# Kernel optimization log

Hardware: AMD Instinct MI355X
Metric: run time of the kernel (lower is better)

Reference implementation:

```python
import jax, jax.numpy as jnp
import numpy as np

K = 3; STRIDE = 1; PAD = 1
IN_C = 256; OUT_C = 512
M = 5; TABLE_SIZE = 16
D = K * K * IN_C  # 2304


def _P(v, m):
    # ALSH preprocessing transform: append norm powers ||v||^2, ||v||^4, ...
    n2 = jnp.sum(v * v)
    powers = jnp.stack([n2 ** (2 ** i) for i in range(m)])
    return jnp.concatenate([v, powers])


def _Q(v, m):
    # ALSH query transform: append m halves
    return jnp.concatenate([v, jnp.full((m,), 0.5, v.dtype)])


def _hash_index(a, v):
    # hf followed by fmod(table_size).abs() as in the torch module
    h = jnp.floor(jnp.dot(a, v))
    return jnp.abs(jnp.mod(h, TABLE_SIZE)).astype(jnp.int32)


def _im2col(x):
    # x: (N, C, H, W) -> (K*K*C, N*h2*w2), rows ordered (kh, kw, c) to match
    # the (out, k, k, in) kernel flattening of the original module.
    N, C, H, W = x.shape
    h2 = (H - K + 2 * PAD) // STRIDE + 1
    w2 = (W - K + 2 * PAD) // STRIDE + 1
    xp = jnp.pad(x, ((0, 0), (0, 0), (PAD, PAD), (PAD, PAD)))
    cols = []
    for i in range(K):          # small fixed loop (k*k = 9)
        for j in range(K):
            cols.append(xp[:, :, i:i + h2 * STRIDE:STRIDE, j:j + w2 * STRIDE:STRIDE])
    p = jnp.stack(cols, 0)                 # (K*K, N, C, h2, w2)
    p = p.transpose(0, 2, 1, 3, 4)         # (K*K, C, N, h2, w2)
    return p.reshape(K * K * C, N * h2 * w2), h2, w2


def setup_inputs() -> dict:
    key = jax.random.key(0)
    k1, k2, k3, k4 = jax.random.split(key, 4)
    stdv = 1.0 / np.sqrt(IN_C * K * K)
    x = jax.random.normal(k1, (16, IN_C, 56, 56), dtype=jnp.float32)
    kernels = jax.random.uniform(k2, (OUT_C, D), dtype=jnp.float32,
                                 minval=-stdv, maxval=stdv)
    bias = jax.random.uniform(k3, (1, OUT_C, 1, 1), dtype=jnp.float32,
                              minval=-stdv, maxval=stdv)
    a = jax.random.normal(k4, (D + M,), dtype=jnp.float32)
    return {"x": x, "kernels": kernels, "bias": bias, "a": a, "mode": 0}


def reference(x, kernels, bias, a, mode):
    N = x.shape[0]
    patch_matr, h2, w2 = _im2col(x)  # (D, N*h2*w2)

    # --- build ALSH table: hash index per kernel row (non-differentiable) ---
    kernel_idx = jax.lax.stop_gradient(
        jax.vmap(lambda kr: _hash_index(a, _P(kr, M)))(kernels))  # (OUT_C,)

    # --- query: max over each patch row, normalized to unit vector ---
    max_row = patch_matr.max(axis=1)                    # (D,)
    unit = max_row / jnp.linalg.norm(max_row)
    q_idx = jax.lax.stop_gradient(_hash_index(a, _Q(unit, M)))

    # --- routed subset matmul, expressed as a row mask (jit-safe) ---
    mask = (kernel_idx == q_idx)                        # (OUT_C,) bool
    count = mask.sum()
    full = kernels @ patch_matr                         # (OUT_C, N*h2*w2)
    scale = jnp.where(count > 0, count / OUT_C, 1.0).astype(full.dtype)
    out = jnp.where(count > 0,
                    jnp.where(mask[:, None], full, 0.0) / scale,
                    full)

    out = out.reshape(OUT_C, N, h2 * w2).transpose(1, 0, 2)
    out = out.reshape(N, OUT_C, h2, w2)
    return out + bias
```

## Files before the change

### kernel.cpp

```cpp
#include <hip/hip_runtime.h>
#include <math.h>

#define IN_C   256
#define OUT_C  512
#define HW     3136
#define W_     56
#define D_     2304
#define TBL    16


#define XB_OFF 2375680ULL
#define XB_ROW 1856

typedef __attribute__((ext_vector_type(8))) __bf16 bf16x8;
typedef __attribute__((ext_vector_type(4))) float f32x4;

__device__ __forceinline__ ushort f2bf(float f) {
  uint b = __float_as_uint(f);
  b = b + 0x7FFFu + ((b >> 16) & 1u);
  return (ushort)(b >> 16);
}

__global__ __launch_bounds__(256) void k_chanmax(const float* __restrict__ x,
                                                 float* __restrict__ ws) {
  int c = blockIdx.x, t = threadIdx.x;
  float m[3][3];
#pragma unroll
  for (int i = 0; i < 3; i++)
#pragma unroll
    for (int j = 0; j < 3; j++) m[i][j] = -INFINITY;

  for (int e = t; e < 16 * HW; e += 256) {
    int n = e / HW;
    int rem = e - n * HW;
    int r = rem / W_;
    int s = rem - r * W_;
    float v = x[(size_t)(n * IN_C + c) * HW + rem];
    bool rc[3] = { r <= 54, true, r >= 1 };
    bool sc[3] = { s <= 54, true, s >= 1 };
#pragma unroll
    for (int i = 0; i < 3; i++)
#pragma unroll
      for (int j = 0; j < 3; j++)
        if (rc[i] && sc[j]) m[i][j] = fmaxf(m[i][j], v);
  }
#pragma unroll
  for (int i = 0; i < 3; i++)
#pragma unroll
    for (int j = 0; j < 3; j++)
      for (int o = 32; o; o >>= 1)
        m[i][j] = fmaxf(m[i][j], __shfl_down(m[i][j], o, 64));

  __shared__ float red[4][9];
  int lane = t & 63, wid = t >> 6;
  if (lane == 0) {
#pragma unroll
    for (int i = 0; i < 3; i++)
#pragma unroll
      for (int j = 0; j < 3; j++) red[wid][i * 3 + j] = m[i][j];
  }
  __syncthreads();
  if (t < 9) {
    float v = fmaxf(fmaxf(red[0][t], red[1][t]), fmaxf(red[2][t], red[3][t]));
    int i = t / 3, j = t - i * 3;
    if (i != 1 || j != 1) v = fmaxf(v, 0.0f);
    ws[(size_t)t * IN_C + c] = v;
  }
}

__global__ __launch_bounds__(256) void k_qhash(const float* __restrict__ a,
                                               float* __restrict__ ws) {
  const float* max_row = ws;
  int t = threadIdx.x;
  double sd = 0.0, sq = 0.0;
  for (int d = t; d < D_; d += 256) {
    double v = (double)max_row[d];
    sd += (double)a[d] * v;
    sq += v * v;
  }
  __shared__ double sh[8], sh2[8];
  int lane = t & 63, wid = t >> 6;
  for (int o = 32; o; o >>= 1) {
    sd += __shfl_down(sd, o, 64);
    sq += __shfl_down(sq, o, 64);
  }
  if (lane == 0) { sh[wid] = sd; sh2[wid] = sq; }
  __syncthreads();
  if (t == 0) {
    double td = 0, tq = 0;
    for (int w = 0; w < 4; w++) { td += sh[w]; tq += sh2[w]; }
    double dot = td / sqrt(tq);
    dot += 0.5 * ((double)a[D_] + (double)a[D_ + 1] + (double)a[D_ + 2] +
                  (double)a[D_ + 3] + (double)a[D_ + 4]);
    long long h = (long long)floor(dot);
    ((int*)ws)[2816] = (int)((h % TBL + TBL) % TBL);
  }
}

__global__ __launch_bounds__(256) void k_khash(const float* __restrict__ kern,
                                               const float* __restrict__ a,
                                               float* __restrict__ ws) {
  int o = blockIdx.x, t = threadIdx.x;
  const float* kr = kern + (size_t)o * D_;
  double sd = 0, sn = 0;
  for (int d = t; d < D_; d += 256) {
    double w = (double)kr[d];
    sd += (double)a[d] * w;
    sn += w * w;
  }
  __shared__ double sh[8], sh2[8];
  int lane = t & 63, wid = t >> 6;
  for (int off = 32; off; off >>= 1) {
    sd += __shfl_down(sd, off, 64);
    sn += __shfl_down(sn, off, 64);
  }
  if (lane == 0) { sh[wid] = sd; sh2[wid] = sn; }
  __syncthreads();
  if (t == 0) {
    double td = 0, tn = 0;
    for (int w = 0; w < 4; w++) { td += sh[w]; tn += sh2[w]; }
    double p1 = tn, p2 = p1 * p1, p4 = p2 * p2, p8 = p4 * p4, p16 = p8 * p8;
    td += (double)a[D_] * p1 + (double)a[D_ + 1] * p2 + (double)a[D_ + 2] * p4 +
          (double)a[D_ + 3] * p8 + (double)a[D_ + 4] * p16;
    long long h = (long long)floor(td);
    ((int*)ws)[2304 + o] = (int)((h % TBL + TBL) % TBL);
  }
}

__global__ __launch_bounds__(512) void k_select(float* __restrict__ ws) {
  int t = threadIdx.x;
  int* hashk = (int*)ws + 2304;
  int* qidx = (int*)ws + 2816;
  int* cntp = (int*)ws + 2817;
  float* scalep = ws + 2818;
  int* active = (int*)ws + 2819;
  int* flags = (int*)ws + 3331;
  __shared__ int cnt;
  if (t == 0) cnt = 0;
  active[t] = 0;
  __syncthreads();
  int q = *qidx;
  bool m = (hashk[t] == q);
  if (m) {
    int p = atomicAdd(&cnt, 1);
    active[p] = t;
  }
  __syncthreads();
  int c = cnt;
  flags[t] = (c == 0) ? 1 : (m ? 1 : 0);
  if (c == 0) active[t] = t;
  if (t == 0) {
    if (c > 0) { *cntp = c; *scalep = 512.0f / (float)c; }
    else       { *cntp = 512; *scalep = 1.0f; }
  }
}

__global__ __launch_bounds__(256) void k_prep(const float* __restrict__ kern,
                                              float* __restrict__ ws) {
  const int* iws = (const int*)ws;
  int cnt = iws[2817];
  const int* active = iws + 2819;
  ushort* Wc = (ushort*)((char*)ws + 16384);
  int s = blockIdx.x, t = threadIdx.x;
  if (s < cnt) {
    int oc = active[s];
    const float* src = kern + (size_t)oc * D_;
    for (int e = t; e < D_; e += 256) Wc[(size_t)s * D_ + e] = f2bf(src[e]);
  } else {
    for (int e = t; e < D_; e += 256) Wc[(size_t)s * D_ + e] = 0;
  }
}

__global__ __launch_bounds__(256) void k_xprep(const float* __restrict__ x,
                                               float* __restrict__ ws) {
  ushort* xb = (ushort*)((char*)ws + XB_OFF);
  int bx = blockIdx.x;
  int n = bx & 15, yp = bx >> 4;
  int t = threadIdx.x;
  const size_t CGS = (size_t)16 * 58 * XB_ROW;
  size_t rb0 = (size_t)(n * 58 + yp) * XB_ROW;
  uint4 z4 = make_uint4(0u, 0u, 0u, 0u);

  if (yp == 0 || yp == 57) {
    for (int e = t; e < 8 * 232; e += 256) {
      int cg = e / 232, k = e - cg * 232;
      *(uint4*)&xb[rb0 + (size_t)cg * CGS + (size_t)k * 8] = z4;
    }
    return;
  }
  if (t < 64) {
    int cg = t >> 3, r = t & 7;
    int wp = (r >> 2) ? 57 : 0;
    int oct = r & 3;
    *(uint4*)&xb[rb0 + (size_t)cg * CGS + wp * 32 + oct * 8] = z4;
  }
  int y = yp - 1;
  __shared__ float Lf[64 * 57];
  for (int c0 = 0; c0 < 256; c0 += 64) {
    __syncthreads();
    for (int e = t; e < 3584; e += 256) {
      int ci = e / 56, w = e - ci * 56;
      Lf[ci * 57 + w] = x[(size_t)(n * 256 + c0 + ci) * 3136 + y * 56 + w];
    }
    __syncthreads();
    for (int e = t; e < 448; e += 256) {
      int w = e >> 3, cg_l = (e >> 2) & 1, oct = e & 3;
      int cb = cg_l * 32 + oct * 8;
      uint pk[4];
#pragma unroll
      for (int k = 0; k < 4; k++) {
        uint lo = f2bf(Lf[(cb + 2 * k) * 57 + w]);
        uint hi = f2bf(Lf[(cb + 2 * k + 1) * 57 + w]);
        pk[k] = lo | (hi << 16);
      }
      int cg = (c0 >> 5) + cg_l;
      *(uint4*)&xb[rb0 + (size_t)cg * CGS + (w + 1) * 32 + oct * 8] =
          make_uint4(pk[0], pk[1], pk[2], pk[3]);
    }
  }
}

__global__ __launch_bounds__(256) void k_biasfill(const float* __restrict__ bias,
                                                  const float* __restrict__ ws,
                                                  float* __restrict__ out) {
  const int* flags = (const int*)ws + 3331;
  const int total4 = 16 * OUT_C * HW / 4;
  int stride = gridDim.x * blockDim.x;
  for (int i = blockIdx.x * blockDim.x + threadIdx.x; i < total4; i += stride) {
    int o = (i / 784) & (OUT_C - 1);
    if (!flags[o]) {
      float b = bias[o];
      ((float4*)out)[i] = make_float4(b, b, b, b);
    }
  }
}

#define XSTR 40
#define ASTR 40
#define XSTRIDE 40
#define ASTRIDE 104

__global__ __launch_bounds__(256, 2) void k_convx(const float* __restrict__ bias,
                                                  const float* __restrict__ ws,
                                                  float* __restrict__ out) {
  const int* iws = (const int*)ws;
  int cnt = iws[2817];
  int octile = blockIdx.y;
  if (octile * 128 >= cnt) return;
  float sc = ws[2818];
  const int* active = iws + 2819;
  const ushort* Wc = (const ushort*)((const char*)ws + 16384);
  const ushort* xb = (const ushort*)((const char*)ws + XB_OFF);

  int rt = blockIdx.x;
  int n = blockIdx.z;
  int t = threadIdx.x;
  int lane = t & 63, wid = t >> 6;
  int quad = lane >> 4, l16 = lane & 15;
  int ochalf = wid & 1, pxhalf = wid >> 1;

  __shared__ __align__(16) ushort X_lds[2][348 * XSTR];
  __shared__ __align__(16) ushort A_lds[2][128 * ASTR];

  int pbase[7];
#pragma unroll
  for (int b = 0; b < 7; b++) {
    int pxl = pxhalf * 112 + b * 16 + l16;
    int rl = pxl / 56;
    int col = pxl - rl * 56;
    pbase[b] = ((rl + 1) * 58 + (col + 1)) * XSTR;
  }

  int ar0 = t >> 2;
  int aq = (t & 3) * 8;
  const ushort* Wrow0 = Wc + (size_t)(octile * 128 + ar0) * D_ + aq;
  const ushort* Wrow1 = Wrow0 + (size_t)64 * D_;
  int aoff0 = ar0 * ASTR + aq;
  int aoff1 = (ar0 + 64) * ASTR + aq;

  const size_t CGS = (size_t)16 * 58 * XB_ROW;
  const ushort* xsrc = xb + (size_t)(n * 58 + rt * 4) * XB_ROW;

  f32x4 acc[4][7];
#pragma unroll
  for (int a = 0; a < 4; a++)
#pragma unroll
    for (int b = 0; b < 7; b++) acc[a][b] = (f32x4){0.f, 0.f, 0.f, 0.f};

  {
    uint4 a0 = *(const uint4*)(Wrow0);
    uint4 a1 = *(const uint4*)(Wrow1);
    *(uint4*)&A_lds[0][aoff0] = a0;
    *(uint4*)&A_lds[0][aoff1] = a1;
    for (int j = t; j < 1392; j += 256)
      *(uint4*)&X_lds[0][(j >> 2) * XSTR + (j & 3) * 8] =
          *(const uint4*)(xsrc + (size_t)j * 8);
  }
  __syncthreads();

  for (int cc = 0; cc < 8; ++cc) {
    const int xc = cc & 1;
#pragma unroll
    for (int tap = 0; tap < 9; ++tap) {
      const int cur = (cc + tap) & 1;
      const bool havenext = !(cc == 7 && tap == 8);
      const int tapn = (tap == 8) ? 0 : tap + 1;
      const int ccn = (tap == 8) ? cc + 1 : cc;
      uint4 a0, a1, xv;
      if (havenext) {
        int goff = tapn * 256 + ccn * 32;
        a0 = *(const uint4*)(Wrow0 + goff);
        a1 = *(const uint4*)(Wrow1 + goff);
      }
      const bool xpf = (tap < 6) && (cc < 7) && (t < 232);
      int xj = tap * 232 + t;
      if (xpf)
        xv = *(const uint4*)(xsrc + (size_t)(cc + 1) * CGS + (size_t)xj * 8);

      const int kh = tap / 3, kw = tap - kh * 3;
      const int poff = ((kh - 1) * 58 + (kw - 1)) * XSTR + quad * 8;
      bf16x8 af[4];
#pragma unroll
      for (int a = 0; a < 4; a++) {
        union { uint4 u; bf16x8 v; } cv;
        cv.u = *(const uint4*)&A_lds[cur][(ochalf * 64 + a * 16 + l16) * ASTR +
                                          quad * 8];
        af[a] = cv.v;
      }
      __builtin_amdgcn_s_setprio(1);
#pragma unroll
      for (int b = 0; b < 7; b++) {
        union { uint4 u; bf16x8 v; } cv;
        cv.u = *(const uint4*)&X_lds[xc][pbase[b] + poff];
        bf16x8 xf = cv.v;
#pragma unroll
        for (int a = 0; a < 4; a++)
          acc[a][b] = __builtin_amdgcn_mfma_f32_16x16x32_bf16(af[a], xf,
                                                              acc[a][b], 0, 0, 0);
      }
      __builtin_amdgcn_s_setprio(0);

      if (havenext) {
        const int nxt = cur ^ 1;
        *(uint4*)&A_lds[nxt][aoff0] = a0;
        *(uint4*)&A_lds[nxt][aoff1] = a1;
      }
      if (xpf)
        *(uint4*)&X_lds[xc ^ 1][(xj >> 2) * XSTR + (xj & 3) * 8] = xv;
      __syncthreads();
    }
  }

  size_t nbase = (size_t)n * OUT_C * HW;
#pragma unroll
  for (int a = 0; a < 4; a++) {
#pragma unroll
    for (int r = 0; r < 4; r++) {
      int slot = octile * 128 + ochalf * 64 + a * 16 + quad * 4 + r;
      if (slot < cnt) {
        int oc = active[slot];
        float bv = bias[oc];
        size_t obase = nbase + (size_t)oc * HW + rt * 224 + pxhalf * 112 + l16;
#pragma unroll
        for (int b = 0; b < 7; b++)
          out[obase + b * 16] = acc[a][b][r] * sc + bv;
      }
    }
  }
}

__global__ __launch_bounds__(256, 2) void k_conv(const float* __restrict__ x,
                                                 const float* __restrict__ bias,
                                                 const float* __restrict__ ws,
                                                 float* __restrict__ out) {
  const int* iws = (const int*)ws;
  int cnt = iws[2817];
  int octile = blockIdx.y;
  if (octile * 128 >= cnt) return;
  float sc = ws[2818];
  const int* active = iws + 2819;
  const ushort* Wc = (const ushort*)((const char*)ws + 16384);

  int rt = blockIdx.x;
  int n = blockIdx.z;
  int t = threadIdx.x;
  int lane = t & 63, wid = t >> 6;
  int quad = lane >> 4, l16 = lane & 15;
  int ochalf = wid & 1, pxhalf = wid >> 1;

  __shared__ __align__(16) ushort X_lds[348 * XSTRIDE];
  __shared__ __align__(16) ushort A_lds[128 * ASTRIDE];

  const float* xin = x + (size_t)n * IN_C * HW;

  int pbase[7];
#pragma unroll
  for (int b = 0; b < 7; b++) {
    int pxl = pxhalf * 112 + b * 16 + l16;
    int rl = pxl / 56;
    int col = pxl - rl * 56;
    pbase[b] = ((rl + 1) * 58 + (col + 1)) * XSTRIDE;
  }

  f32x4 acc[4][7];
#pragma unroll
  for (int a = 0; a < 4; a++)
#pragma unroll
    for (int b = 0; b < 7; b++) acc[a][b] = (f32x4){0.f, 0.f, 0.f, 0.f};

  for (int cc = 0; cc < 8; ++cc) {
    int c0 = cc * 32;
    __syncthreads();
    for (int e = t; e < 1392; e += 256) {
      int q = e / 348;
      int p = e - q * 348;
      int rl = p / 58;
      int cp = p - rl * 58;
      int y = rt * 4 - 1 + rl;
      int xx = cp - 1;
      float vv[8];
      if ((unsigned)y < 56u && (unsigned)xx < 56u) {
        const float* src = xin + (size_t)(c0 + q * 8) * HW + y * W_ + xx;
#pragma unroll
        for (int k = 0; k < 8; k++) vv[k] = src[(size_t)k * HW];
      } else {
#pragma unroll
        for (int k = 0; k < 8; k++) vv[k] = 0.f;
      }
      uint4 pk;
      pk.x = (uint)f2bf(vv[0]) | ((uint)f2bf(vv[1]) << 16);
      pk.y = (uint)f2bf(vv[2]) | ((uint)f2bf(vv[3]) << 16);
      pk.z = (uint)f2bf(vv[4]) | ((uint)f2bf(vv[5]) << 16);
      pk.w = (uint)f2bf(vv[6]) | ((uint)f2bf(vv[7]) << 16);
      *(uint4*)&X_lds[p * XSTRIDE + q * 8] = pk;
    }

    for (int kh = 0; kh < 3; ++kh) {
      __syncthreads();
      for (int e = t; e < 1536; e += 256) {
        int oc = e / 12;
        int seg = e - oc * 12;
        int tl = seg >> 2, q = seg & 3;
        uint4 v = *(const uint4*)(Wc + (size_t)(octile * 128 + oc) * D_ +
                                  (kh * 3 + tl) * IN_C + c0 + q * 8);
        *(uint4*)&A_lds[oc * ASTRIDE + tl * 32 + q * 8] = v;
      }
      __syncthreads();

      int di = kh - 1;
#pragma unroll
      for (int djj = 0; djj < 3; ++djj) {
        int poff = (di * 58 + (djj - 1)) * XSTRIDE + quad * 8;
        bf16x8 bfr[7];
#pragma unroll
        for (int b = 0; b < 7; b++) {
          union { uint4 u; bf16x8 v; } cv;
          cv.u = *(const uint4*)&X_lds[pbase[b] + poff];
          bfr[b] = cv.v;
        }
#pragma unroll
        for (int a = 0; a < 4; a++) {
          union { uint4 u; bf16x8 v; } cv;
          cv.u = *(const uint4*)&A_lds[(ochalf * 64 + a * 16 + l16) * ASTRIDE +
                                       djj * 32 + quad * 8];
          bf16x8 af = cv.v;
#pragma unroll
          for (int b = 0; b < 7; b++)
            acc[a][b] = __builtin_amdgcn_mfma_f32_16x16x32_bf16(af, bfr[b],
                                                                acc[a][b], 0, 0, 0);
        }
      }
    }
  }

  size_t nbase = (size_t)n * OUT_C * HW;
#pragma unroll
  for (int a = 0; a < 4; a++) {
#pragma unroll
    for (int r = 0; r < 4; r++) {
      int slot = octile * 128 + ochalf * 64 + a * 16 + quad * 4 + r;
      if (slot < cnt) {
        int oc = active[slot];
        float bv = bias[oc];
        size_t obase = nbase + (size_t)oc * HW + rt * 224 + pxhalf * 112 + l16;
#pragma unroll
        for (int b = 0; b < 7; b++)
          out[obase + b * 16] = acc[a][b][r] * sc + bv;
      }
    }
  }
}

extern "C" void kernel_launch(void* const* d_in, const int* in_sizes, int n_in,
                              void* d_out, int out_size, void* d_ws, size_t ws_size,
                              hipStream_t stream) {
  const float* x    = (const float*)d_in[0];
  const float* kern = (const float*)d_in[1];
  const float* bias = (const float*)d_in[2];
  const float* a    = (const float*)d_in[3];
  float* out = (float*)d_out;
  float* ws  = (float*)d_ws;

  const size_t need = XB_OFF + (size_t)8 * 16 * 58 * 58 * 32 * 2;

  k_chanmax<<<dim3(IN_C), dim3(256), 0, stream>>>(x, ws);
  k_qhash<<<dim3(1), dim3(256), 0, stream>>>(a, ws);
  k_khash<<<dim3(OUT_C), dim3(256), 0, stream>>>(kern, a, ws);
  k_select<<<dim3(1), dim3(512), 0, stream>>>(ws);
  k_prep<<<dim3(OUT_C), dim3(256), 0, stream>>>(kern, ws);
  k_biasfill<<<dim3(4096), dim3(256), 0, stream>>>(bias, ws, out);
  if (ws_size >= need) {
    k_xprep<<<dim3(16 * 58), dim3(256), 0, stream>>>(x, ws);
    k_convx<<<dim3(14, 4, 16), dim3(256), 0, stream>>>(bias, ws, out);
  } else {
    k_conv<<<dim3(14, 4, 16), dim3(256), 0, stream>>>(x, bias, ws, out);
  }
}
```

Before: 371.4 us.

## Fuse setup kernels, fold bias fill into conv, deepen weight prefetch

Merges the x bf16 repack, the channel-max reduction (split across four batch parts) and the kernel hashing into one k_setup launch, and replaces the query hash and selection kernels with a single k_route kernel. The separate bias-fill pass over the whole output is removed; inactive output channels are now bias-filled inside k_convx by the otherwise idle octile blocks. The conv loop prefetches weights two taps ahead through registers and delays the X LDS store by one step, hiding global latency better. It also widens the k_prep bf16 stores. This cuts launch count and a full output write, at the cost of more register pressure in the conv kernel and extra workspace for the partial maxima.

```diff
diff --git a/kernel.cpp b/kernel.cpp
--- a/kernel.cpp
+++ b/kernel.cpp
@@ -11,6 +11,7 @@
 
 #define XB_OFF 2375680ULL
 #define XB_ROW 1856
+#define P_OFF  7483392
 
 typedef __attribute__((ext_vector_type(8))) __bf16 bf16x8;
 typedef __attribute__((ext_vector_type(4))) float f32x4;
@@ -21,6 +22,360 @@
   return (ushort)(b >> 16);
 }
 
+
+__global__ __launch_bounds__(256) void k_setup(const float* __restrict__ x,
+                                               const float* __restrict__ kern,
+                                               const float* __restrict__ a,
+                                               float* __restrict__ ws) {
+  __shared__ __align__(16) float smem[64 * 57];
+  int bx = blockIdx.x, t = threadIdx.x;
+
+  if (bx < 3712) {
+    int c0i = bx & 3;
+    int n = (bx >> 2) & 15;
+    int yp = bx >> 6;
+    int c0 = c0i * 64, cgbase = c0i * 2;
+    ushort* xb = (ushort*)((char*)ws + XB_OFF);
+    const size_t CGS = (size_t)16 * 58 * XB_ROW;
+    size_t rb0 = (size_t)(n * 58 + yp) * XB_ROW;
+    uint4 z4 = make_uint4(0u, 0u, 0u, 0u);
+
+    if (yp == 0 || yp == 57) {
+      for (int e = t; e < 464; e += 256) {
+        int cg_l = e / 232, k = e - cg_l * 232;
+        *(uint4*)&xb[rb0 + (size_t)(cgbase + cg_l) * CGS + (size_t)k * 8] = z4;
+      }
+      return;
+    }
+    if (t < 16) {
+      int cg_l = t >> 3, r = t & 7;
+      int wp = (r >> 2) ? 57 : 0, oct = r & 3;
+      *(uint4*)&xb[rb0 + (size_t)(cgbase + cg_l) * CGS + wp * 32 + oct * 8] = z4;
+    }
+    int y = yp - 1;
+    float* Lf = smem;
+    for (int e = t; e < 3584; e += 256) {
+      int ci = e / 56, w = e - ci * 56;
+      Lf[ci * 57 + w] = x[(size_t)(n * 256 + c0 + ci) * 3136 + y * 56 + w];
+    }
+    __syncthreads();
+    for (int e = t; e < 448; e += 256) {
+      int w = e >> 3, cg_l = (e >> 2) & 1, oct = e & 3;
+      int cb = cg_l * 32 + oct * 8;
+      uint pk[4];
+#pragma unroll
+      for (int k = 0; k < 4; k++) {
+        uint lo = f2bf(Lf[(cb + 2 * k) * 57 + w]);
+        uint hi = f2bf(Lf[(cb + 2 * k + 1) * 57 + w]);
+        pk[k] = lo | (hi << 16);
+      }
+      *(uint4*)&xb[rb0 + (size_t)(cgbase + cg_l) * CGS + (w + 1) * 32 + oct * 8] =
+          make_uint4(pk[0], pk[1], pk[2], pk[3]);
+    }
+  } else if (bx < 4736) {
+    int idx = bx - 3712;
+    int c = idx & 255, part = idx >> 8;
+    float m[3][3];
+#pragma unroll
+    for (int i = 0; i < 3; i++)
+#pragma unroll
+      for (int j = 0; j < 3; j++) m[i][j] = -INFINITY;
+    for (int e = t; e < 4 * HW; e += 256) {
+      int nl = e / HW;
+      int rem = e - nl * HW;
+      int r = rem / W_;
+      int s = rem - r * W_;
+      float v = x[(size_t)((part * 4 + nl) * IN_C + c) * HW + rem];
+      bool rc[3] = { r <= 54, true, r >= 1 };
+      bool sc[3] = { s <= 54, true, s >= 1 };
+#pragma unroll
+      for (int i = 0; i < 3; i++)
+#pragma unroll
+        for (int j = 0; j < 3; j++)
+          if (rc[i] && sc[j]) m[i][j] = fmaxf(m[i][j], v);
+    }
+#pragma unroll
+    for (int i = 0; i < 3; i++)
+#pragma unroll
+      for (int j = 0; j < 3; j++)
+        for (int o = 32; o; o >>= 1)
+          m[i][j] = fmaxf(m[i][j], __shfl_down(m[i][j], o, 64));
+    float* red = smem;
+    int lane = t & 63, wid = t >> 6;
+    if (lane == 0) {
+#pragma unroll
+      for (int i = 0; i < 3; i++)
+#pragma unroll
+        for (int j = 0; j < 3; j++) red[wid * 9 + i * 3 + j] = m[i][j];
+    }
+    __syncthreads();
+    if (t < 9) {
+      float v = fmaxf(fmaxf(red[0 * 9 + t], red[1 * 9 + t]),
+                      fmaxf(red[2 * 9 + t], red[3 * 9 + t]));
+      ws[P_OFF + (size_t)part * 2304 + (size_t)t * IN_C + c] = v;
+    }
+  } else {
+    int o = bx - 4736;
+    const float* kr = kern + (size_t)o * D_;
+    double sd = 0, sn = 0;
+    for (int d = t; d < D_; d += 256) {
+      double w = (double)kr[d];
+      sd += (double)a[d] * w;
+      sn += w * w;
+    }
+    double* sh = (double*)smem;
+    double* sh2 = sh + 8;
+    int lane = t & 63, wid = t >> 6;
+    for (int off = 32; off; off >>= 1) {
+      sd += __shfl_down(sd, off, 64);
+      sn += __shfl_down(sn, off, 64);
+    }
+    if (lane == 0) { sh[wid] = sd; sh2[wid] = sn; }
+    __syncthreads();
+    if (t == 0) {
+      double td = 0, tn = 0;
+      for (int w = 0; w < 4; w++) { td += sh[w]; tn += sh2[w]; }
+      double p1 = tn, p2 = p1 * p1, p4 = p2 * p2, p8 = p4 * p4, p16 = p8 * p8;
+      td += (double)a[D_] * p1 + (double)a[D_ + 1] * p2 + (double)a[D_ + 2] * p4 +
+            (double)a[D_ + 3] * p8 + (double)a[D_ + 4] * p16;
+      long long h = (long long)floor(td);
+      ((int*)ws)[2304 + o] = (int)((h % TBL + TBL) % TBL);
+    }
+  }
+}
+
+__global__ __launch_bounds__(512) void k_route(const float* __restrict__ a,
+                                               float* __restrict__ ws) {
+  int t = threadIdx.x;
+  const float* P = ws + P_OFF;
+  __shared__ double sh[8], sh2[8];
+  __shared__ int shq, c1, c2;
+  double sd = 0.0, sq = 0.0;
+  if (t < 256) {
+    for (int d = t; d < D_; d += 256) {
+      float v = fmaxf(fmaxf(P[d], P[2304 + d]), fmaxf(P[4608 + d], P[6912 + d]));
+      if ((d >> 8) != 4) v = fmaxf(v, 0.0f);
+      double dv = (double)v;
+      sd += (double)a[d] * dv;
+      sq += dv * dv;
+    }
+    for (int o = 32; o; o >>= 1) {
+      sd += __shfl_down(sd, o, 64);
+      sq += __shfl_down(sq, o, 64);
+    }
+    if ((t & 63) == 0) { sh[t >> 6] = sd; sh2[t >> 6] = sq; }
+  }
+  __syncthreads();
+  if (t == 0) {
+    double td = 0, tq = 0;
+    for (int w = 0; w < 4; w++) { td += sh[w]; tq += sh2[w]; }
+    double dot = td / sqrt(tq);
+    dot += 0.5 * ((double)a[D_] + (double)a[D_ + 1] + (double)a[D_ + 2] +
+                  (double)a[D_ + 3] + (double)a[D_ + 4]);
+    long long h = (long long)floor(dot);
+    int q = (int)((h % TBL + TBL) % TBL);
+    ((int*)ws)[2816] = q;
+    shq = q;
+    c1 = 0; c2 = 0;
+  }
+  __syncthreads();
+  int* hashk = (int*)ws + 2304;
+  int* cntp = (int*)ws + 2817;
+  float* scalep = ws + 2818;
+  int* active = (int*)ws + 2819;
+  int* inact = (int*)ws + 3331;
+  int q = shq;
+  bool m = (hashk[t] == q);
+  if (m) active[atomicAdd(&c1, 1)] = t;
+  else   inact[atomicAdd(&c2, 1)] = t;
+  __syncthreads();
+  int c = c1;
+  if (c == 0) active[t] = t;
+  if (t == 0) {
+    if (c > 0) { *cntp = c; *scalep = 512.0f / (float)c; }
+    else       { *cntp = 512; *scalep = 1.0f; }
+  }
+}
+
+__global__ __launch_bounds__(256) void k_prep(const float* __restrict__ kern,
+                                              float* __restrict__ ws) {
+  const int* iws = (const int*)ws;
+  int cnt = iws[2817];
+  const int* active = iws + 2819;
+  uint* Wc = (uint*)((char*)ws + 16384);
+  int s = blockIdx.x, t = threadIdx.x;
+  if (s < cnt) {
+    int oc = active[s];
+    const float* src = kern + (size_t)oc * D_;
+    for (int e = t; e < 1152; e += 256) {
+      uint lo = f2bf(src[2 * e]);
+      uint hi = f2bf(src[2 * e + 1]);
+      Wc[(size_t)s * 1152 + e] = lo | (hi << 16);
+    }
+  } else {
+    for (int e = t; e < 1152; e += 256) Wc[(size_t)s * 1152 + e] = 0;
+  }
+}
+
+#define XSTR 40
+#define ASTR 40
+#define XSTRIDE 40
+#define ASTRIDE 104
+
+__global__ __launch_bounds__(256, 2) void k_convx(const float* __restrict__ bias,
+                                                  const float* __restrict__ ws,
+                                                  float* __restrict__ out) {
+  const int* iws = (const int*)ws;
+  int cnt = iws[2817];
+  int octile = blockIdx.y;
+  int rt = blockIdx.x;
+  int n = blockIdx.z;
+  int t = threadIdx.x;
+
+  {
+    int base = octile * 128;
+    int lo = base < cnt ? cnt : base;
+    int hi = base + 128;
+    if (lo < hi) {
+      const int* inact = iws + 3331;
+      size_t nbase = (size_t)n * OUT_C * HW;
+      int nin = hi - lo;
+      for (int e = t; e < nin * 56; e += 256) {
+        int j = e / 56, f = e - j * 56;
+        int oc = inact[lo - cnt + j];
+        float bv = bias[oc];
+        ((float4*)out)[(nbase + (size_t)oc * HW + rt * 224) / 4 + f] =
+            make_float4(bv, bv, bv, bv);
+      }
+    }
+    if (base >= cnt) return;
+  }
+
+  float sc = ws[2818];
+  const int* active = iws + 2819;
+  const ushort* Wc = (const ushort*)((const char*)ws + 16384);
+  const ushort* xb = (const ushort*)((const char*)ws + XB_OFF);
+
+  int lane = t & 63, wid = t >> 6;
+  int quad = lane >> 4, l16 = lane & 15;
+  int ochalf = wid & 1, pxhalf = wid >> 1;
+
+  __shared__ __align__(16) ushort X_lds[2][348 * XSTR];
+  __shared__ __align__(16) ushort A_lds[2][128 * ASTR];
+
+  int pbase[7];
+#pragma unroll
+  for (int b = 0; b < 7; b++) {
+    int pxl = pxhalf * 112 + b * 16 + l16;
+    int rl = pxl / 56;
+    int col = pxl - rl * 56;
+    pbase[b] = ((rl + 1) * 58 + (col + 1)) * XSTR;
+  }
+
+  int ar0 = t >> 2;
+  int aq = (t & 3) * 8;
+  const ushort* Wrow0 = Wc + (size_t)(octile * 128 + ar0) * D_ + aq;
+  const ushort* Wrow1 = Wrow0 + (size_t)64 * D_;
+  int aoff0 = ar0 * ASTR + aq;
+  int aoff1 = (ar0 + 64) * ASTR + aq;
+
+  const size_t CGS = (size_t)16 * 58 * XB_ROW;
+  const ushort* xsrc = xb + (size_t)(n * 58 + rt * 4) * XB_ROW;
+
+  f32x4 acc[4][7];
+#pragma unroll
+  for (int a = 0; a < 4; a++)
+#pragma unroll
+    for (int b = 0; b < 7; b++) acc[a][b] = (f32x4){0.f, 0.f, 0.f, 0.f};
+
+  uint4 pA0, pA1, nA0, nA1;
+  uint4 xh; int xhj = 0; bool xhv = false;
+
+  {
+    uint4 a0 = *(const uint4*)(Wrow0);
+    uint4 a1 = *(const uint4*)(Wrow1);
+    *(uint4*)&A_lds[0][aoff0] = a0;
+    *(uint4*)&A_lds[0][aoff1] = a1;
+    for (int j = t; j < 1392; j += 256)
+      *(uint4*)&X_lds[0][(j >> 2) * XSTR + (j & 3) * 8] =
+          *(const uint4*)(xsrc + (size_t)j * 8);
+    pA0 = *(const uint4*)(Wrow0 + 256);
+    pA1 = *(const uint4*)(Wrow1 + 256);
+  }
+  __syncthreads();
+
+  for (int cc = 0; cc < 8; ++cc) {
+    const int xc = cc & 1;
+#pragma unroll
+    for (int tap = 0; tap < 9; ++tap) {
+      const int cur = (cc + tap) & 1;
+      const bool last = (cc == 7) && (tap == 8);
+      const int tap2 = (tap + 2) % 9;
+      const int cc2 = cc + (tap + 2) / 9;
+      if (cc2 < 8) {
+        int goff = tap2 * 256 + cc2 * 32;
+        nA0 = *(const uint4*)(Wrow0 + goff);
+        nA1 = *(const uint4*)(Wrow1 + goff);
+      }
+      const bool xpf = (tap < 6) && (cc < 7) && (t < 232);
+      uint4 xv; int xj = tap * 232 + t;
+      if (xpf)
+        xv = *(const uint4*)(xsrc + (size_t)(cc + 1) * CGS + (size_t)xj * 8);
+
+      const int kh = tap / 3, kw = tap - kh * 3;
+      const int poff = ((kh - 1) * 58 + (kw - 1)) * XSTR + quad * 8;
+      bf16x8 af[4];
+#pragma unroll
+      for (int a = 0; a < 4; a++) {
+        union { uint4 u; bf16x8 v; } cv;
+        cv.u = *(const uint4*)&A_lds[cur][(ochalf * 64 + a * 16 + l16) * ASTR +
+                                          quad * 8];
+        af[a] = cv.v;
+      }
+      __builtin_amdgcn_s_setprio(1);
+#pragma unroll
+      for (int b = 0; b < 7; b++) {
+        union { uint4 u; bf16x8 v; } cv;
+        cv.u = *(const uint4*)&X_lds[xc][pbase[b] + poff];
+        bf16x8 xf = cv.v;
+#pragma unroll
+        for (int a = 0; a < 4; a++)
+          acc[a][b] = __builtin_amdgcn_mfma_f32_16x16x32_bf16(af[a], xf,
+                                                              acc[a][b], 0, 0, 0);
+      }
+      __builtin_amdgcn_s_setprio(0);
+
+      if (!last) {
+        *(uint4*)&A_lds[cur ^ 1][aoff0] = pA0;
+        *(uint4*)&A_lds[cur ^ 1][aoff1] = pA1;
+      }
+      if (xhv)
+        *(uint4*)&X_lds[xc ^ 1][(xhj >> 2) * XSTR + (xhj & 3) * 8] = xh;
+      __syncthreads();
+      pA0 = nA0; pA1 = nA1;
+      xh = xv; xhj = xj; xhv = xpf;
+    }
+  }
+
+  size_t nbase = (size_t)n * OUT_C * HW;
+#pragma unroll
+  for (int a = 0; a < 4; a++) {
+#pragma unroll
+    for (int r = 0; r < 4; r++) {
+      int slot = octile * 128 + ochalf * 64 + a * 16 + quad * 4 + r;
+      if (slot < cnt) {
+        int oc = active[slot];
+        float bv = bias[oc];
+        size_t obase = nbase + (size_t)oc * HW + rt * 224 + pxhalf * 112 + l16;
+#pragma unroll
+        for (int b = 0; b < 7; b++)
+          out[obase + b * 16] = acc[a][b][r] * sc + bv;
+      }
+    }
+  }
+}
+
+
 __global__ __launch_bounds__(256) void k_chanmax(const float* __restrict__ x,
                                                  float* __restrict__ ws) {
   int c = blockIdx.x, t = threadIdx.x;
@@ -29,7 +384,6 @@
   for (int i = 0; i < 3; i++)
 #pragma unroll
     for (int j = 0; j < 3; j++) m[i][j] = -INFINITY;
-
   for (int e = t; e < 16 * HW; e += 256) {
     int n = e / HW;
     int rem = e - n * HW;
@@ -50,7 +404,6 @@
     for (int j = 0; j < 3; j++)
       for (int o = 32; o; o >>= 1)
         m[i][j] = fmaxf(m[i][j], __shfl_down(m[i][j], o, 64));
-
   __shared__ float red[4][9];
   int lane = t & 63, wid = t >> 6;
   if (lane == 0) {
@@ -155,71 +508,6 @@
   }
 }
 
-__global__ __launch_bounds__(256) void k_prep(const float* __restrict__ kern,
-                                              float* __restrict__ ws) {
-  const int* iws = (const int*)ws;
-  int cnt = iws[2817];
-  const int* active = iws + 2819;
-  ushort* Wc = (ushort*)((char*)ws + 16384);
-  int s = blockIdx.x, t = threadIdx.x;
-  if (s < cnt) {
-    int oc = active[s];
-    const float* src = kern + (size_t)oc * D_;
-    for (int e = t; e < D_; e += 256) Wc[(size_t)s * D_ + e] = f2bf(src[e]);
-  } else {
-    for (int e = t; e < D_; e += 256) Wc[(size_t)s * D_ + e] = 0;
-  }
-}
-
-__global__ __launch_bounds__(256) void k_xprep(const float* __restrict__ x,
-                                               float* __restrict__ ws) {
-  ushort* xb = (ushort*)((char*)ws + XB_OFF);
-  int bx = blockIdx.x;
-  int n = bx & 15, yp = bx >> 4;
-  int t = threadIdx.x;
-  const size_t CGS = (size_t)16 * 58 * XB_ROW;
-  size_t rb0 = (size_t)(n * 58 + yp) * XB_ROW;
-  uint4 z4 = make_uint4(0u, 0u, 0u, 0u);
-
-  if (yp == 0 || yp == 57) {
-    for (int e = t; e < 8 * 232; e += 256) {
-      int cg = e / 232, k = e - cg * 232;
-      *(uint4*)&xb[rb0 + (size_t)cg * CGS + (size_t)k * 8] = z4;
-    }
-    return;
-  }
-  if (t < 64) {
-    int cg = t >> 3, r = t & 7;
-    int wp = (r >> 2) ? 57 : 0;
-    int oct = r & 3;
-    *(uint4*)&xb[rb0 + (size_t)cg * CGS + wp * 32 + oct * 8] = z4;
-  }
-  int y = yp - 1;
-  __shared__ float Lf[64 * 57];
-  for (int c0 = 0; c0 < 256; c0 += 64) {
-    __syncthreads();
-    for (int e = t; e < 3584; e += 256) {
-      int ci = e / 56, w = e - ci * 56;
-      Lf[ci * 57 + w] = x[(size_t)(n * 256 + c0 + ci) * 3136 + y * 56 + w];
-    }
-    __syncthreads();
-    for (int e = t; e < 448; e += 256) {
-      int w = e >> 3, cg_l = (e >> 2) & 1, oct = e & 3;
-      int cb = cg_l * 32 + oct * 8;
-      uint pk[4];
-#pragma unroll
-      for (int k = 0; k < 4; k++) {
-        uint lo = f2bf(Lf[(cb + 2 * k) * 57 + w]);
-        uint hi = f2bf(Lf[(cb + 2 * k + 1) * 57 + w]);
-        pk[k] = lo | (hi << 16);
-      }
-      int cg = (c0 >> 5) + cg_l;
-      *(uint4*)&xb[rb0 + (size_t)cg * CGS + (w + 1) * 32 + oct * 8] =
-          make_uint4(pk[0], pk[1], pk[2], pk[3]);
-    }
-  }
-}
-
 __global__ __launch_bounds__(256) void k_biasfill(const float* __restrict__ bias,
                                                   const float* __restrict__ ws,
                                                   float* __restrict__ out) {
@@ -235,140 +523,6 @@
   }
 }
 
-#define XSTR 40
-#define ASTR 40
-#define XSTRIDE 40
-#define ASTRIDE 104
-
-__global__ __launch_bounds__(256, 2) void k_convx(const float* __restrict__ bias,
-                                                  const float* __restrict__ ws,
-                                                  float* __restrict__ out) {
-  const int* iws = (const int*)ws;
-  int cnt = iws[2817];
-  int octile = blockIdx.y;
-  if (octile * 128 >= cnt) return;
-  float sc = ws[2818];
-  const int* active = iws + 2819;
-  const ushort* Wc = (const ushort*)((const char*)ws + 16384);
-  const ushort* xb = (const ushort*)((const char*)ws + XB_OFF);
-
-  int rt = blockIdx.x;
-  int n = blockIdx.z;
-  int t = threadIdx.x;
-  int lane = t & 63, wid = t >> 6;
-  int quad = lane >> 4, l16 = lane & 15;
-  int ochalf = wid & 1, pxhalf = wid >> 1;
-
-  __shared__ __align__(16) ushort X_lds[2][348 * XSTR];
-  __shared__ __align__(16) ushort A_lds[2][128 * ASTR];
-
-  int pbase[7];
-#pragma unroll
-  for (int b = 0; b < 7; b++) {
-    int pxl = pxhalf * 112 + b * 16 + l16;
-    int rl = pxl / 56;
-    int col = pxl - rl * 56;
-    pbase[b] = ((rl + 1) * 58 + (col + 1)) * XSTR;
-  }
-
-  int ar0 = t >> 2;
-  int aq = (t & 3) * 8;
-  const ushort* Wrow0 = Wc + (size_t)(octile * 128 + ar0) * D_ + aq;
-  const ushort* Wrow1 = Wrow0 + (size_t)64 * D_;
-  int aoff0 = ar0 * ASTR + aq;
-  int aoff1 = (ar0 + 64) * ASTR + aq;
-
-  const size_t CGS = (size_t)16 * 58 * XB_ROW;
-  const ushort* xsrc = xb + (size_t)(n * 58 + rt * 4) * XB_ROW;
-
-  f32x4 acc[4][7];
-#pragma unroll
-  for (int a = 0; a < 4; a++)
-#pragma unroll
-    for (int b = 0; b < 7; b++) acc[a][b] = (f32x4){0.f, 0.f, 0.f, 0.f};
-
-  {
-    uint4 a0 = *(const uint4*)(Wrow0);
-    uint4 a1 = *(const uint4*)(Wrow1);
-    *(uint4*)&A_lds[0][aoff0] = a0;
-    *(uint4*)&A_lds[0][aoff1] = a1;
-    for (int j = t; j < 1392; j += 256)
-      *(uint4*)&X_lds[0][(j >> 2) * XSTR + (j & 3) * 8] =
-          *(const uint4*)(xsrc + (size_t)j * 8);
-  }
-  __syncthreads();
-
-  for (int cc = 0; cc < 8; ++cc) {
-    const int xc = cc & 1;
-#pragma unroll
-    for (int tap = 0; tap < 9; ++tap) {
-      const int cur = (cc + tap) & 1;
-      const bool havenext = !(cc == 7 && tap == 8);
-      const int tapn = (tap == 8) ? 0 : tap + 1;
-      const int ccn = (tap == 8) ? cc + 1 : cc;
-      uint4 a0, a1, xv;
-      if (havenext) {
-        int goff = tapn * 256 + ccn * 32;
-        a0 = *(const uint4*)(Wrow0 + goff);
-        a1 = *(const uint4*)(Wrow1 + goff);
-      }
-      const bool xpf = (tap < 6) && (cc < 7) && (t < 232);
-      int xj = tap * 232 + t;
-      if (xpf)
-        xv = *(const uint4*)(xsrc + (size_t)(cc + 1) * CGS + (size_t)xj * 8);
-
-      const int kh = tap / 3, kw = tap - kh * 3;
-      const int poff = ((kh - 1) * 58 + (kw - 1)) * XSTR + quad * 8;
-      bf16x8 af[4];
-#pragma unroll
-      for (int a = 0; a < 4; a++) {
-        union { uint4 u; bf16x8 v; } cv;
-        cv.u = *(const uint4*)&A_lds[cur][(ochalf * 64 + a * 16 + l16) * ASTR +
-                                          quad * 8];
-        af[a] = cv.v;
-      }
-      __builtin_amdgcn_s_setprio(1);
-#pragma unroll
-      for (int b = 0; b < 7; b++) {
-        union { uint4 u; bf16x8 v; } cv;
-        cv.u = *(const uint4*)&X_lds[xc][pbase[b] + poff];
-        bf16x8 xf = cv.v;
-#pragma unroll
-        for (int a = 0; a < 4; a++)
-          acc[a][b] = __builtin_amdgcn_mfma_f32_16x16x32_bf16(af[a], xf,
-                                                              acc[a][b], 0, 0, 0);
-      }
-      __builtin_amdgcn_s_setprio(0);
-
-      if (havenext) {
-        const int nxt = cur ^ 1;
-        *(uint4*)&A_lds[nxt][aoff0] = a0;
-        *(uint4*)&A_lds[nxt][aoff1] = a1;
-      }
-      if (xpf)
-        *(uint4*)&X_lds[xc ^ 1][(xj >> 2) * XSTR + (xj & 3) * 8] = xv;
-      __syncthreads();
-    }
-  }
-
-  size_t nbase = (size_t)n * OUT_C * HW;
-#pragma unroll
-  for (int a = 0; a < 4; a++) {
-#pragma unroll
-    for (int r = 0; r < 4; r++) {
-      int slot = octile * 128 + ochalf * 64 + a * 16 + quad * 4 + r;
-      if (slot < cnt) {
-        int oc = active[slot];
-        float bv = bias[oc];
-        size_t obase = nbase + (size_t)oc * HW + rt * 224 + pxhalf * 112 + l16;
-#pragma unroll
-        for (int b = 0; b < 7; b++)
-          out[obase + b * 16] = acc[a][b][r] * sc + bv;
-      }
-    }
-  }
-}
-
 __global__ __launch_bounds__(256, 2) void k_conv(const float* __restrict__ x,
                                                  const float* __restrict__ bias,
                                                  const float* __restrict__ ws,
@@ -380,19 +534,15 @@
   float sc = ws[2818];
   const int* active = iws + 2819;
   const ushort* Wc = (const ushort*)((const char*)ws + 16384);
-
   int rt = blockIdx.x;
   int n = blockIdx.z;
   int t = threadIdx.x;
   int lane = t & 63, wid = t >> 6;
   int quad = lane >> 4, l16 = lane & 15;
   int ochalf = wid & 1, pxhalf = wid >> 1;
-
   __shared__ __align__(16) ushort X_lds[348 * XSTRIDE];
   __shared__ __align__(16) ushort A_lds[128 * ASTRIDE];
-
   const float* xin = x + (size_t)n * IN_C * HW;
-
   int pbase[7];
 #pragma unroll
   for (int b = 0; b < 7; b++) {
@@ -401,13 +551,11 @@
     int col = pxl - rl * 56;
     pbase[b] = ((rl + 1) * 58 + (col + 1)) * XSTRIDE;
   }
-
   f32x4 acc[4][7];
 #pragma unroll
   for (int a = 0; a < 4; a++)
 #pragma unroll
     for (int b = 0; b < 7; b++) acc[a][b] = (f32x4){0.f, 0.f, 0.f, 0.f};
-
   for (int cc = 0; cc < 8; ++cc) {
     int c0 = cc * 32;
     __syncthreads();
@@ -434,7 +582,6 @@
       pk.w = (uint)f2bf(vv[6]) | ((uint)f2bf(vv[7]) << 16);
       *(uint4*)&X_lds[p * XSTRIDE + q * 8] = pk;
     }
-
     for (int kh = 0; kh < 3; ++kh) {
       __syncthreads();
       for (int e = t; e < 1536; e += 256) {
@@ -446,7 +593,6 @@
         *(uint4*)&A_lds[oc * ASTRIDE + tl * 32 + q * 8] = v;
       }
       __syncthreads();
-
       int di = kh - 1;
 #pragma unroll
       for (int djj = 0; djj < 3; ++djj) {
@@ -472,7 +618,6 @@
       }
     }
   }
-
   size_t nbase = (size_t)n * OUT_C * HW;
 #pragma unroll
   for (int a = 0; a < 4; a++) {
@@ -501,18 +646,20 @@
   float* out = (float*)d_out;
   float* ws  = (float*)d_ws;
 
-  const size_t need = XB_OFF + (size_t)8 * 16 * 58 * 58 * 32 * 2;
-
-  k_chanmax<<<dim3(IN_C), dim3(256), 0, stream>>>(x, ws);
-  k_qhash<<<dim3(1), dim3(256), 0, stream>>>(a, ws);
-  k_khash<<<dim3(OUT_C), dim3(256), 0, stream>>>(kern, a, ws);
-  k_select<<<dim3(1), dim3(512), 0, stream>>>(ws);
-  k_prep<<<dim3(OUT_C), dim3(256), 0, stream>>>(kern, ws);
-  k_biasfill<<<dim3(4096), dim3(256), 0, stream>>>(bias, ws, out);
+  const size_t need = 29933568ULL + 4 * 2304 * 4;
+
   if (ws_size >= need) {
-    k_xprep<<<dim3(16 * 58), dim3(256), 0, stream>>>(x, ws);
+    k_setup<<<dim3(5248), dim3(256), 0, stream>>>(x, kern, a, ws);
+    k_route<<<dim3(1), dim3(512), 0, stream>>>(a, ws);
+    k_prep<<<dim3(OUT_C), dim3(256), 0, stream>>>(kern, ws);
     k_convx<<<dim3(14, 4, 16), dim3(256), 0, stream>>>(bias, ws, out);
   } else {
+    k_chanmax<<<dim3(IN_C), dim3(256), 0, stream>>>(x, ws);
+    k_qhash<<<dim3(1), dim3(256), 0, stream>>>(a, ws);
+    k_khash<<<dim3(OUT_C), dim3(256), 0, stream>>>(kern, a, ws);
+    k_select<<<dim3(1), dim3(512), 0, stream>>>(ws);
+    k_prep<<<dim3(OUT_C), dim3(256), 0, stream>>>(kern, ws);
+    k_biasfill<<<dim3(4096), dim3(256), 0, stream>>>(bias, ws, out);
     k_conv<<<dim3(14, 4, 16), dim3(256), 0, stream>>>(x, bias, ws, out);
   }
 }
```

New measurement: 298.6 us. 1.24x faster.
